# Optimization experiments

Hardware: AMD Instinct MI355X
Metric: run time of the kernel (lower is better)

## Reference

```python
import jax, jax.numpy as jnp
import numpy as np
import math

B, S, D = 4, 2048, 768
H = 12
DH = D // H  # 64
NEG = -1e10

def setup_inputs() -> dict:
    key = jax.random.key(0)
    ks = jax.random.split(key, 8)
    scale = 0.02
    return {
        "hidden_states": jax.random.normal(ks[0], (B, S, D), dtype=jnp.float32),
        "attention_mask": jnp.zeros((B, 1, 1, S), dtype=jnp.float32),
        "Wq": jax.random.normal(ks[1], (D, D), dtype=jnp.float32) * scale,
        "bq": jnp.zeros((D,), dtype=jnp.float32),
        "Wk": jax.random.normal(ks[2], (D, D), dtype=jnp.float32) * scale,
        "bk": jnp.zeros((D,), dtype=jnp.float32),
        "Wv": jax.random.normal(ks[3], (D, D), dtype=jnp.float32) * scale,
        "bv": jnp.zeros((D,), dtype=jnp.float32),
    }

def reference(hidden_states, attention_mask, Wq, bq, Wk, bk, Wv, bv):
    # Linear projections; note attention_mask is accepted but unused, matching the torch module.
    def split_heads(x):  # [B,S,D] -> [B,H,S,DH]
        return x.reshape(B, S, H, DH).transpose(0, 2, 1, 3)
    q = split_heads(hidden_states @ Wq + bq)
    k = split_heads(hidden_states @ Wk + bk)
    v = split_heads(hidden_states @ Wv + bv)
    scores = jnp.einsum("bhqd,bhkd->bhqk", q, k) / math.sqrt(DH)
    causal = jnp.tril(jnp.ones((S, S), dtype=bool))  # masked_fill(mask==0, -1e10)
    scores = jnp.where(causal, scores, NEG)
    probs = jax.nn.softmax(scores, axis=-1)
    # dropout prob = 0.0 (eval) -> identity
    ctx = jnp.einsum("bhqk,bhkd->bhqd", probs, v)
    return ctx.transpose(0, 2, 1, 3).reshape(B, S, D)
```

## Files before the change

### kernel.cpp

```cpp
#include <hip/hip_runtime.h>
#include <hip/hip_bf16.h>

#define B_  4
#define S_  2048
#define D_  768
#define H_  12
#define DH_ 64

typedef __bf16 bf16;
typedef __attribute__((ext_vector_type(8))) __bf16 bf16x8;
typedef __attribute__((ext_vector_type(4))) __bf16 bf16x4;
typedef __attribute__((ext_vector_type(4))) float floatx4;
typedef __attribute__((ext_vector_type(16))) float floatx16;

__device__ __forceinline__ void load_lds16(const bf16* g, bf16* l) {
    __builtin_amdgcn_global_load_lds((const __attribute__((address_space(1))) void*)g,
                                     (__attribute__((address_space(3))) void*)l, 16, 0, 0);
}

__device__ __forceinline__ unsigned pack2(float a, float b) {
    unsigned ua = __builtin_bit_cast(unsigned, a) + 0x8000u;
    unsigned ub = __builtin_bit_cast(unsigned, b) + 0x8000u;
    return __builtin_amdgcn_perm(ub, ua, 0x07060302);
}

__device__ __forceinline__ int chunk_off2(int qt2) {
    if (qt2 < 4)  return qt2;
    if (qt2 < 8)  return 4 + 2 * (qt2 - 4);
    if (qt2 < 12) return 12 + 3 * (qt2 - 8);
    return 24 + 4 * (qt2 - 12);
}

__global__ __launch_bounds__(256) void cvt_f32_bf16(const float* __restrict__ in,
                                                    bf16* __restrict__ out, int n4) {
    int i = blockIdx.x * 256 + threadIdx.x;
    if (i < n4) {
        float4 v = ((const float4*)in)[i];
        bf16x4 o;
        o[0] = (bf16)v.x; o[1] = (bf16)v.y; o[2] = (bf16)v.z; o[3] = (bf16)v.w;
        *(bf16x4*)(out + (size_t)i * 4) = o;
    }
}

__global__ __launch_bounds__(256) void w_transpose(const float* __restrict__ w0,
                                                   const float* __restrict__ w1,
                                                   const float* __restrict__ w2,
                                                   bf16* __restrict__ Wt)
{
    const int which = blockIdx.z;
    const float* W = (which == 0) ? w0 : (which == 1 ? w1 : w2);
    bf16* dst = Wt + (size_t)which * D_ * D_;
    __shared__ bf16 t[64 * 72];
    const int k0 = blockIdx.x * 64, n0 = blockIdx.y * 64;
    const int tid = threadIdx.x;
    {
        int r = tid >> 2;
        int c0 = (tid & 3) * 16;
        #pragma unroll
        for (int q = 0; q < 4; q++) {
            float4 v = *(const float4*)(W + (size_t)(k0 + r) * D_ + n0 + c0 + q * 4);
            t[(c0 + q * 4 + 0) * 72 + r] = (bf16)v.x;
            t[(c0 + q * 4 + 1) * 72 + r] = (bf16)v.y;
            t[(c0 + q * 4 + 2) * 72 + r] = (bf16)v.z;
            t[(c0 + q * 4 + 3) * 72 + r] = (bf16)v.w;
        }
    }
    __syncthreads();
    {
        int n = tid >> 3, seg = tid & 7;
        *(bf16x8*)(dst + (size_t)(n0 + n) * D_ + k0 + seg * 8) =
            *(const bf16x8*)(t + n * 72 + seg * 8);
        *(bf16x8*)(dst + (size_t)(n0 + n + 32) * D_ + k0 + seg * 8) =
            *(const bf16x8*)(t + (n + 32) * 72 + seg * 8);
    }
}

__global__ __launch_bounds__(256) void qkv_gemm(
    const bf16* __restrict__ Xb, const bf16* __restrict__ Wt,
    const float* __restrict__ bq, const float* __restrict__ bk,
    const float* __restrict__ bv, bf16* __restrict__ QKV)
{
    const int which = blockIdx.z;
    const bf16* Wm = Wt + (size_t)which * D_ * D_;
    const float* bias = (which == 0) ? bq : (which == 1 ? bk : bv);
    bf16* out = QKV + (size_t)which * B_ * H_ * S_ * DH_;

    __shared__ bf16 As[2][128 * 64];
    __shared__ bf16 Bs[2][128 * 64];

    const int tid  = threadIdx.x;
    const int wave = tid >> 6, lane = tid & 63;
    const int wr = wave >> 1, wc = wave & 1;
    const int l31 = lane & 31, lh = lane >> 5;
    const int m0 = blockIdx.x * 128, n0 = blockIdx.y * 128;

    int row_[4], off_[4], lds_[4];
    #pragma unroll
    for (int i = 0; i < 4; i++) {
        int fc = i * 256 + tid;
        int row = fc >> 3;
        row_[i] = row;
        off_[i] = ((fc & 7) ^ (row & 7)) * 8;
        lds_[i] = fc * 8;
    }

    floatx16 acc[2][2];
    #pragma unroll
    for (int mt = 0; mt < 2; mt++)
        #pragma unroll
        for (int nt = 0; nt < 2; nt++)
            #pragma unroll
            for (int e = 0; e < 16; e++) acc[mt][nt][e] = 0.f;

    #pragma unroll
    for (int i = 0; i < 4; i++) {
        load_lds16(Xb + (size_t)(m0 + row_[i]) * D_ + off_[i], &As[0][lds_[i]]);
        load_lds16(Wm + (size_t)(n0 + row_[i]) * D_ + off_[i], &Bs[0][lds_[i]]);
    }

    const int rxor = l31 & 7;
    for (int it = 0; it < 12; ++it) {
        const int cur = it & 1;
        __syncthreads();
        if (it + 1 < 12) {
            const int kn = (it + 1) * 64;
            #pragma unroll
            for (int i = 0; i < 4; i++) {
                load_lds16(Xb + (size_t)(m0 + row_[i]) * D_ + kn + off_[i], &As[cur ^ 1][lds_[i]]);
                load_lds16(Wm + (size_t)(n0 + row_[i]) * D_ + kn + off_[i], &Bs[cur ^ 1][lds_[i]]);
            }
        }
        const bf16* Ac = As[cur];
        const bf16* Bc = Bs[cur];
        #pragma unroll
        for (int s = 0; s < 4; s++) {
            const int sx = (((s << 1) | lh) ^ rxor) << 3;
            bf16x8 af[2], bfr[2];
            #pragma unroll
            for (int mt = 0; mt < 2; mt++)
                af[mt] = *(const bf16x8*)(Ac + ((wr * 64 + mt * 32 + l31) << 6) + sx);
            #pragma unroll
            for (int nt = 0; nt < 2; nt++)
                bfr[nt] = *(const bf16x8*)(Bc + ((wc * 64 + nt * 32 + l31) << 6) + sx);
            #pragma unroll
            for (int mt = 0; mt < 2; mt++)
                #pragma unroll
                for (int nt = 0; nt < 2; nt++)
                    acc[mt][nt] = __builtin_amdgcn_mfma_f32_32x32x16_bf16(
                        af[mt], bfr[nt], acc[mt][nt], 0, 0, 0);
        }
    }

    const float sc = (which == 0) ? 0.125f : 1.0f;
    #pragma unroll
    for (int mt = 0; mt < 2; mt++) {
        #pragma unroll
        for (int nt = 0; nt < 2; nt++) {
            const int n = n0 + wc * 64 + nt * 32 + l31;
            const float bv_ = bias[n];
            const int h = n >> 6, dh = n & 63;
            const int mb = m0 + wr * 64 + mt * 32 + 4 * lh;
            #pragma unroll
            for (int rq = 0; rq < 4; rq++) {
                const int m = mb + 8 * rq;
                const int b = m >> 11, s0 = m & 2047;
                if (which == 2) {
                    bf16x4 o;
                    #pragma unroll
                    for (int rr = 0; rr < 4; rr++) o[rr] = (bf16)(acc[mt][nt][4 * rq + rr] + bv_);
                    *(bf16x4*)(out + ((size_t)((b * H_ + h) * DH_ + dh)) * S_ + s0) = o;
                } else {
                    #pragma unroll
                    for (int rr = 0; rr < 4; rr++)
                        out[(((size_t)(b * H_ + h) * S_ + s0 + rr) << 6) + dh] =
                            (bf16)((acc[mt][nt][4 * rq + rr] + bv_) * sc);
                }
            }
        }
    }
}

__global__ __launch_bounds__(256) void attn_chunk(const bf16* __restrict__ QKV,
                                                  float* __restrict__ out,
                                                  bf16* __restrict__ Opart,
                                                  float* __restrict__ Lpart)
{
    const int cid = 39 - blockIdx.x;
    const int bh = blockIdx.y;
    const int b = bh / H_, h = bh % H_;

    int qt2, c;
    if (cid < 4)       { qt2 = cid; c = 0; }
    else if (cid < 12) { int t = cid - 4;  qt2 = 4 + (t >> 1);  c = t & 1; }
    else if (cid < 24) { int t = cid - 12; qt2 = 8 + t / 3;     c = t - 3 * (t / 3); }
    else               { int t = cid - 24; qt2 = 12 + (t >> 2); c = t & 3; }
    const int nch = (2 * qt2 + 9) >> 3;
    const int kt0 = c * 8;
    const int kt1 = min(kt0 + 7, 2 * qt2 + 1);

    const size_t MAT = (size_t)B_ * H_ * S_ * DH_;
    const bf16* Q  = QKV +           (size_t)bh * S_ * DH_;
    const bf16* K  = QKV + MAT +     (size_t)bh * S_ * DH_;
    const bf16* Vt = QKV + 2 * MAT + (size_t)bh * S_ * DH_;

    __shared__ bf16 Ks[2][64 * 64];
    __shared__ bf16 Vs[2][64 * 64];

    const int tid  = threadIdx.x;
    const int wave = tid >> 6, lane = tid & 63;
    const int l31 = lane & 31, lh = lane >> 5;
    const int qbase = qt2 * 128;
    const int qs = qbase + wave * 32;
    const int q = qs + l31;

    int srow_[2], soff_[2], slds_[2];
    #pragma unroll
    for (int i = 0; i < 2; i++) {
        int fc = i * 256 + tid;
        int row = fc >> 3;
        srow_[i] = row;
        soff_[i] = ((fc & 7) ^ (row & 7)) * 8;
        slds_[i] = fc * 8;
    }

    bf16x8 qf[4];
    {
        const bf16* qrow = Q + (size_t)q * DH_ + lh * 8;
        #pragma unroll
        for (int s = 0; s < 4; s++) qf[s] = *(const bf16x8*)(qrow + s * 16);
    }

    floatx16 accO[2];
    #pragma unroll
    for (int dt = 0; dt < 2; dt++)
        #pragma unroll
        for (int e = 0; e < 16; e++) accO[dt][e] = 0.f;
    float lsum[4] = {0.f, 0.f, 0.f, 0.f};

    #pragma unroll
    for (int i = 0; i < 2; i++) {
        load_lds16(K + ((size_t)(kt0 * 64 + srow_[i]) << 6) + soff_[i], &Ks[0][slds_[i]]);
        load_lds16(Vt + (size_t)srow_[i] * S_ + kt0 * 64 + soff_[i], &Vs[0][slds_[i]]);
    }

    const int rxor = l31 & 7;
    for (int kt = kt0; kt <= kt1; ++kt) {
        const int cur = (kt - kt0) & 1;
        __syncthreads();
        if (kt < kt1) {
            #pragma unroll
            for (int i = 0; i < 2; i++) {
                load_lds16(K + ((size_t)((kt + 1) * 64 + srow_[i]) << 6) + soff_[i],
                           &Ks[cur ^ 1][slds_[i]]);
                load_lds16(Vt + (size_t)srow_[i] * S_ + (kt + 1) * 64 + soff_[i],
                           &Vs[cur ^ 1][slds_[i]]);
            }
        }
        const bf16* Kc = Ks[cur];
        const bf16* Vc = Vs[cur];

        const bool domask = (kt * 64 + 63 > qs);

        #pragma unroll
        for (int kk = 0; kk < 2; kk++) {
            floatx16 accS;
            #pragma unroll
            for (int e = 0; e < 16; e++) accS[e] = 0.f;
            #pragma unroll
            for (int s = 0; s < 4; s++) {
                const int sx = (((s << 1) | lh) ^ rxor) << 3;
                bf16x8 kf = *(const bf16x8*)(Kc + ((kk * 32 + l31) << 6) + sx);
                accS = __builtin_amdgcn_mfma_f32_32x32x16_bf16(kf, qf[s], accS, 0, 0, 0);
            }

            unsigned pk1[4], pk2[4];
            if (domask) {
                const int keyb = kt * 64 + kk * 32 + 4 * lh;
                #pragma unroll
                for (int rq = 0; rq < 4; rq++) {
                    float p[4];
                    #pragma unroll
                    for (int rr = 0; rr < 4; rr++) {
                        float v = __expf(accS[4 * rq + rr]);
                        if (keyb + 8 * rq + rr > q) v = 0.f;
                        p[rr] = v;
                        lsum[rq] += v;
                    }
                    pk1[rq] = pack2(p[0], p[1]);
                    pk2[rq] = pack2(p[2], p[3]);
                }
            } else {
                #pragma unroll
                for (int rq = 0; rq < 4; rq++) {
                    float p[4];
                    #pragma unroll
                    for (int rr = 0; rr < 4; rr++) {
                        float v = __expf(accS[4 * rq + rr]);
                        p[rr] = v;
                        lsum[rq] += v;
                    }
                    pk1[rq] = pack2(p[0], p[1]);
                    pk2[rq] = pack2(p[2], p[3]);
                }
            }

            #pragma unroll
            for (int sl = 0; sl < 2; sl++) {
                const int s = kk * 2 + sl;
                unsigned sendA = lh ? pk1[2 * sl] : pk1[2 * sl + 1];
                unsigned sendB = lh ? pk2[2 * sl] : pk2[2 * sl + 1];
                unsigned recvA = __shfl_xor(sendA, 32, 64);
                unsigned recvB = __shfl_xor(sendB, 32, 64);
                uint4 w;
                w.x = lh ? recvA : pk1[2 * sl];
                w.y = lh ? recvB : pk2[2 * sl];
                w.z = lh ? pk1[2 * sl + 1] : recvA;
                w.w = lh ? pk2[2 * sl + 1] : recvB;
                bf16x8 ptf = __builtin_bit_cast(bf16x8, w);
                const int sx = (((s << 1) | lh) ^ rxor) << 3;
                #pragma unroll
                for (int dt = 0; dt < 2; dt++) {
                    bf16x8 vf = *(const bf16x8*)(Vc + ((dt * 32 + l31) << 6) + sx);
                    accO[dt] = __builtin_amdgcn_mfma_f32_32x32x16_bf16(vf, ptf, accO[dt], 0, 0, 0);
                }
            }
        }
    }

    const float Lr = (lsum[0] + lsum[1]) + (lsum[2] + lsum[3]);
    const float L = Lr + __shfl_xor(Lr, 32, 64);

    if (nch == 1) {
        const float inv = 1.0f / L;
        float* orow = out + (size_t)(b * S_ + q) * D_ + h * DH_;
        #pragma unroll
        for (int dt = 0; dt < 2; dt++)
            #pragma unroll
            for (int rq = 0; rq < 4; rq++) {
                float4 o;
                o.x = accO[dt][4 * rq + 0] * inv; o.y = accO[dt][4 * rq + 1] * inv;
                o.z = accO[dt][4 * rq + 2] * inv; o.w = accO[dt][4 * rq + 3] * inv;
                *(float4*)(orow + dt * 32 + 8 * rq + 4 * lh) = o;
            }
    } else {
        const int chunk = bh * 40 + chunk_off2(qt2) + c;
        bf16* obase = Opart + (size_t)chunk * 8192 + (wave * 32 + l31) * 64;
        #pragma unroll
        for (int dt = 0; dt < 2; dt++)
            #pragma unroll
            for (int rq = 0; rq < 4; rq++) {
                bf16x4 o;
                #pragma unroll
                for (int rr = 0; rr < 4; rr++) o[rr] = (bf16)accO[dt][4 * rq + rr];
                *(bf16x4*)(obase + dt * 32 + 8 * rq + 4 * lh) = o;
            }
        if (lh == 0) Lpart[chunk * 128 + wave * 32 + l31] = L;
    }
}

__global__ __launch_bounds__(256) void attn_reduce(const bf16* __restrict__ Opart,
                                                   const float* __restrict__ Lpart,
                                                   float* __restrict__ out)
{
    const int qt2 = 4 + blockIdx.x;
    const int bh = blockIdx.y;
    const int b = bh / H_, h = bh % H_;
    const int nch = (2 * qt2 + 9) >> 3;
    const int cb = bh * 40 + chunk_off2(qt2);

    const int e = threadIdx.x;
    const int ql = e >> 1, dh0 = (e & 1) * 32;

    float o[32];
    #pragma unroll
    for (int i = 0; i < 32; i++) o[i] = 0.f;
    float l = 0.f;

    for (int cidx = 0; cidx < nch; cidx++) {
        const bf16* p = Opart + (size_t)(cb + cidx) * 8192 + ql * 64 + dh0;
        #pragma unroll
        for (int m = 0; m < 4; m++) {
            bf16x8 v = *(const bf16x8*)(p + m * 8);
            #pragma unroll
            for (int k = 0; k < 8; k++) o[m * 8 + k] += (float)v[k];
        }
        l += Lpart[(cb + cidx) * 128 + ql];
    }
    float inv = 1.0f / l;
    float* orow = out + (size_t)(b * S_ + qt2 * 128 + ql) * D_ + h * DH_ + dh0;
    #pragma unroll
    for (int m = 0; m < 8; m++) {
        float4 v;
        v.x = o[m * 4 + 0] * inv; v.y = o[m * 4 + 1] * inv;
        v.z = o[m * 4 + 2] * inv; v.w = o[m * 4 + 3] * inv;
        *(float4*)(orow + m * 4) = v;
    }
}

extern "C" void kernel_launch(void* const* d_in, const int* in_sizes, int n_in,
                              void* d_out, int out_size, void* d_ws, size_t ws_size,
                              hipStream_t stream) {
    const float* hs = (const float*)d_in[0];
    const float* Wq = (const float*)d_in[2];
    const float* bq = (const float*)d_in[3];
    const float* Wk = (const float*)d_in[4];
    const float* bk = (const float*)d_in[5];
    const float* Wv = (const float*)d_in[6];
    const float* bv = (const float*)d_in[7];
    float* out = (float*)d_out;

    bf16* Xb    = (bf16*)d_ws;
    bf16* Wt    = Xb + (size_t)8192 * 768;
    bf16* QKV   = Wt + (size_t)3 * 768 * 768;
    bf16* Opart = QKV + (size_t)3 * B_ * H_ * S_ * DH_;
    float* Lpart = (float*)(Opart + (size_t)1920 * 8192);

    cvt_f32_bf16<<<6144, 256, 0, stream>>>(hs, Xb, 1572864);
    w_transpose<<<dim3(12, 12, 3), 256, 0, stream>>>(Wq, Wk, Wv, Wt);
    qkv_gemm<<<dim3(64, 6, 3), 256, 0, stream>>>(Xb, Wt, bq, bk, bv, QKV);
    attn_chunk<<<dim3(40, 48), 256, 0, stream>>>(QKV, out, Opart, Lpart);
    attn_reduce<<<dim3(12, 48), 256, 0, stream>>>(Opart, Lpart, out);
}
```

Baseline: 206.6 us.

## Fuse prep kernels, shrink GEMM K-tile, switch attention to register-staged padded LDS

```diff
diff --git a/kernel.cpp b/kernel.cpp
--- a/kernel.cpp
+++ b/kernel.cpp
@@ -31,28 +31,30 @@
     return 24 + 4 * (qt2 - 12);
 }
 
-__global__ __launch_bounds__(256) void cvt_f32_bf16(const float* __restrict__ in,
-                                                    bf16* __restrict__ out, int n4) {
-    int i = blockIdx.x * 256 + threadIdx.x;
-    if (i < n4) {
-        float4 v = ((const float4*)in)[i];
+__global__ __launch_bounds__(256) void prep(const float* __restrict__ hs,
+                                            const float* __restrict__ w0,
+                                            const float* __restrict__ w1,
+                                            const float* __restrict__ w2,
+                                            bf16* __restrict__ Xb,
+                                            bf16* __restrict__ Wt)
+{
+    __shared__ bf16 t[64 * 72];
+    const int bx = blockIdx.x;
+    const int tid = threadIdx.x;
+    if (bx < 6144) {
+        int i = bx * 256 + tid;
+        float4 v = ((const float4*)hs)[i];
         bf16x4 o;
         o[0] = (bf16)v.x; o[1] = (bf16)v.y; o[2] = (bf16)v.z; o[3] = (bf16)v.w;
-        *(bf16x4*)(out + (size_t)i * 4) = o;
-    }
-}
-
-__global__ __launch_bounds__(256) void w_transpose(const float* __restrict__ w0,
-                                                   const float* __restrict__ w1,
-                                                   const float* __restrict__ w2,
-                                                   bf16* __restrict__ Wt)
-{
-    const int which = blockIdx.z;
+        *(bf16x4*)(Xb + (size_t)i * 4) = o;
+        return;
+    }
+    const int tb = bx - 6144;
+    const int which = tb / 144;
+    const int rest = tb % 144;
+    const int k0 = (rest / 12) * 64, n0 = (rest % 12) * 64;
     const float* W = (which == 0) ? w0 : (which == 1 ? w1 : w2);
     bf16* dst = Wt + (size_t)which * D_ * D_;
-    __shared__ bf16 t[64 * 72];
-    const int k0 = blockIdx.x * 64, n0 = blockIdx.y * 64;
-    const int tid = threadIdx.x;
     {
         int r = tid >> 2;
         int c0 = (tid & 3) * 16;
@@ -85,8 +87,8 @@
     const float* bias = (which == 0) ? bq : (which == 1 ? bk : bv);
     bf16* out = QKV + (size_t)which * B_ * H_ * S_ * DH_;
 
-    __shared__ bf16 As[2][128 * 64];
-    __shared__ bf16 Bs[2][128 * 64];
+    __shared__ bf16 As[2][128 * 32];
+    __shared__ bf16 Bs[2][128 * 32];
 
     const int tid  = threadIdx.x;
     const int wave = tid >> 6, lane = tid & 63;
@@ -94,13 +96,15 @@
     const int l31 = lane & 31, lh = lane >> 5;
     const int m0 = blockIdx.x * 128, n0 = blockIdx.y * 128;
 
-    int row_[4], off_[4], lds_[4];
-    #pragma unroll
-    for (int i = 0; i < 4; i++) {
+    const bf16 *ga_[2], *gb_[2];
+    int lds_[2];
+    #pragma unroll
+    for (int i = 0; i < 2; i++) {
         int fc = i * 256 + tid;
-        int row = fc >> 3;
-        row_[i] = row;
-        off_[i] = ((fc & 7) ^ (row & 7)) * 8;
+        int row = fc >> 2, cpos = fc & 3;
+        int gc = (cpos - (row >> 1)) & 3;
+        ga_[i] = Xb + (size_t)(m0 + row) * D_ + gc * 8;
+        gb_[i] = Wm + (size_t)(n0 + row) * D_ + gc * 8;
         lds_[i] = fc * 8;
     }
 
@@ -113,35 +117,35 @@
             for (int e = 0; e < 16; e++) acc[mt][nt][e] = 0.f;
 
     #pragma unroll
-    for (int i = 0; i < 4; i++) {
-        load_lds16(Xb + (size_t)(m0 + row_[i]) * D_ + off_[i], &As[0][lds_[i]]);
-        load_lds16(Wm + (size_t)(n0 + row_[i]) * D_ + off_[i], &Bs[0][lds_[i]]);
-    }
-
-    const int rxor = l31 & 7;
-    for (int it = 0; it < 12; ++it) {
+    for (int i = 0; i < 2; i++) {
+        load_lds16(ga_[i], &As[0][lds_[i]]);
+        load_lds16(gb_[i], &Bs[0][lds_[i]]);
+    }
+
+    const int cp = (l31 >> 1) & 3;
+    for (int it = 0; it < 24; ++it) {
         const int cur = it & 1;
         __syncthreads();
-        if (it + 1 < 12) {
-            const int kn = (it + 1) * 64;
-            #pragma unroll
-            for (int i = 0; i < 4; i++) {
-                load_lds16(Xb + (size_t)(m0 + row_[i]) * D_ + kn + off_[i], &As[cur ^ 1][lds_[i]]);
-                load_lds16(Wm + (size_t)(n0 + row_[i]) * D_ + kn + off_[i], &Bs[cur ^ 1][lds_[i]]);
+        if (it + 1 < 24) {
+            const int kn = (it + 1) * 32;
+            #pragma unroll
+            for (int i = 0; i < 2; i++) {
+                load_lds16(ga_[i] + kn, &As[cur ^ 1][lds_[i]]);
+                load_lds16(gb_[i] + kn, &Bs[cur ^ 1][lds_[i]]);
             }
         }
         const bf16* Ac = As[cur];
         const bf16* Bc = Bs[cur];
         #pragma unroll
-        for (int s = 0; s < 4; s++) {
-            const int sx = (((s << 1) | lh) ^ rxor) << 3;
+        for (int s = 0; s < 2; s++) {
+            const int off = ((2 * s + lh + cp) & 3) * 8;
             bf16x8 af[2], bfr[2];
             #pragma unroll
             for (int mt = 0; mt < 2; mt++)
-                af[mt] = *(const bf16x8*)(Ac + ((wr * 64 + mt * 32 + l31) << 6) + sx);
+                af[mt] = *(const bf16x8*)(Ac + (wr * 64 + mt * 32 + l31) * 32 + off);
             #pragma unroll
             for (int nt = 0; nt < 2; nt++)
-                bfr[nt] = *(const bf16x8*)(Bc + ((wc * 64 + nt * 32 + l31) << 6) + sx);
+                bfr[nt] = *(const bf16x8*)(Bc + (wc * 64 + nt * 32 + l31) * 32 + off);
             #pragma unroll
             for (int mt = 0; mt < 2; mt++)
                 #pragma unroll
@@ -180,10 +184,10 @@
     }
 }
 
-__global__ __launch_bounds__(256) void attn_chunk(const bf16* __restrict__ QKV,
-                                                  float* __restrict__ out,
-                                                  bf16* __restrict__ Opart,
-                                                  float* __restrict__ Lpart)
+__global__ __launch_bounds__(256, 3) void attn_chunk(const bf16* __restrict__ QKV,
+                                                     float* __restrict__ out,
+                                                     bf16* __restrict__ Opart,
+                                                     float* __restrict__ Lpart)
 {
     const int cid = 39 - blockIdx.x;
     const int bh = blockIdx.y;
@@ -203,26 +207,17 @@
     const bf16* K  = QKV + MAT +     (size_t)bh * S_ * DH_;
     const bf16* Vt = QKV + 2 * MAT + (size_t)bh * S_ * DH_;
 
-    __shared__ bf16 Ks[2][64 * 64];
-    __shared__ bf16 Vs[2][64 * 64];
+    __shared__ bf16 Ks[64 * 72];
+    __shared__ bf16 Vts[64 * 72];
 
     const int tid  = threadIdx.x;
     const int wave = tid >> 6, lane = tid & 63;
     const int l31 = lane & 31, lh = lane >> 5;
+    const int srow = tid >> 3, sseg = tid & 7;
     const int qbase = qt2 * 128;
     const int qs = qbase + wave * 32;
     const int q = qs + l31;
 
-    int srow_[2], soff_[2], slds_[2];
-    #pragma unroll
-    for (int i = 0; i < 2; i++) {
-        int fc = i * 256 + tid;
-        int row = fc >> 3;
-        srow_[i] = row;
-        soff_[i] = ((fc & 7) ^ (row & 7)) * 8;
-        slds_[i] = fc * 8;
-    }
-
     bf16x8 qf[4];
     {
         const bf16* qrow = Q + (size_t)q * DH_ + lh * 8;
@@ -237,27 +232,28 @@
         for (int e = 0; e < 16; e++) accO[dt][e] = 0.f;
     float lsum[4] = {0.f, 0.f, 0.f, 0.f};
 
-    #pragma unroll
-    for (int i = 0; i < 2; i++) {
-        load_lds16(K + ((size_t)(kt0 * 64 + srow_[i]) << 6) + soff_[i], &Ks[0][slds_[i]]);
-        load_lds16(Vt + (size_t)srow_[i] * S_ + kt0 * 64 + soff_[i], &Vs[0][slds_[i]]);
-    }
-
-    const int rxor = l31 & 7;
+    const bf16* kptr = K  + (size_t)(kt0 * 64 + srow) * DH_ + sseg * 8;
+    const bf16* vptr = Vt + (size_t)srow * S_ + kt0 * 64 + sseg * 8;
+    bf16x8 ka = *(const bf16x8*)kptr;
+    bf16x8 kb = *(const bf16x8*)(kptr + 32 * DH_);
+    bf16x8 va = *(const bf16x8*)vptr;
+    bf16x8 vb = *(const bf16x8*)(vptr + (size_t)32 * S_);
+
     for (int kt = kt0; kt <= kt1; ++kt) {
-        const int cur = (kt - kt0) & 1;
+        __syncthreads();
+        *(bf16x8*)(Ks  + srow * 72 + sseg * 8) = ka;
+        *(bf16x8*)(Ks  + (srow + 32) * 72 + sseg * 8) = kb;
+        *(bf16x8*)(Vts + srow * 72 + sseg * 8) = va;
+        *(bf16x8*)(Vts + (srow + 32) * 72 + sseg * 8) = vb;
         __syncthreads();
         if (kt < kt1) {
-            #pragma unroll
-            for (int i = 0; i < 2; i++) {
-                load_lds16(K + ((size_t)((kt + 1) * 64 + srow_[i]) << 6) + soff_[i],
-                           &Ks[cur ^ 1][slds_[i]]);
-                load_lds16(Vt + (size_t)srow_[i] * S_ + (kt + 1) * 64 + soff_[i],
-                           &Vs[cur ^ 1][slds_[i]]);
-            }
-        }
-        const bf16* Kc = Ks[cur];
-        const bf16* Vc = Vs[cur];
+            kptr += 64 * DH_;
+            vptr += 64;
+            ka = *(const bf16x8*)kptr;
+            kb = *(const bf16x8*)(kptr + 32 * DH_);
+            va = *(const bf16x8*)vptr;
+            vb = *(const bf16x8*)(vptr + (size_t)32 * S_);
+        }
 
         const bool domask = (kt * 64 + 63 > qs);
 
@@ -268,8 +264,7 @@
             for (int e = 0; e < 16; e++) accS[e] = 0.f;
             #pragma unroll
             for (int s = 0; s < 4; s++) {
-                const int sx = (((s << 1) | lh) ^ rxor) << 3;
-                bf16x8 kf = *(const bf16x8*)(Kc + ((kk * 32 + l31) << 6) + sx);
+                bf16x8 kf = *(const bf16x8*)(Ks + (kk * 32 + l31) * 72 + s * 16 + lh * 8);
                 accS = __builtin_amdgcn_mfma_f32_32x32x16_bf16(kf, qf[s], accS, 0, 0, 0);
             }
 
@@ -317,10 +312,9 @@
                 w.z = lh ? pk1[2 * sl + 1] : recvA;
                 w.w = lh ? pk2[2 * sl + 1] : recvB;
                 bf16x8 ptf = __builtin_bit_cast(bf16x8, w);
-                const int sx = (((s << 1) | lh) ^ rxor) << 3;
                 #pragma unroll
                 for (int dt = 0; dt < 2; dt++) {
-                    bf16x8 vf = *(const bf16x8*)(Vc + ((dt * 32 + l31) << 6) + sx);
+                    bf16x8 vf = *(const bf16x8*)(Vts + (dt * 32 + l31) * 72 + s * 16 + lh * 8);
                     accO[dt] = __builtin_amdgcn_mfma_f32_32x32x16_bf16(vf, ptf, accO[dt], 0, 0, 0);
                 }
             }
@@ -415,8 +409,7 @@
     bf16* Opart = QKV + (size_t)3 * B_ * H_ * S_ * DH_;
     float* Lpart = (float*)(Opart + (size_t)1920 * 8192);
 
-    cvt_f32_bf16<<<6144, 256, 0, stream>>>(hs, Xb, 1572864);
-    w_transpose<<<dim3(12, 12, 3), 256, 0, stream>>>(Wq, Wk, Wv, Wt);
+    prep<<<6576, 256, 0, stream>>>(hs, Wq, Wk, Wv, Xb, Wt);
     qkv_gemm<<<dim3(64, 6, 3), 256, 0, stream>>>(Xb, Wt, bq, bk, bv, QKV);
     attn_chunk<<<dim3(40, 48), 256, 0, stream>>>(QKV, out, Opart, Lpart);
     attn_reduce<<<dim3(12, 48), 256, 0, stream>>>(Opart, Lpart, out);
```

Measured after the change: 202.5 us. -2.0%, faster.
